# Performance work log

Hardware: AMD Instinct MI355X
Metric: run time of the kernel (lower is better)

The kernel has to match this reference:

```python
import jax, jax.numpy as jnp
import numpy as np
import math

# dims
BSZ, L, D = 2, 4096, 1024
EXPAND, DS, NH, NG, DC, CS = 2, 128, 32, 1, 4, 64
DI = EXPAND * D            # 2048
HP = DI // NH              # 64 headdim
D_IN_PROJ = 2 * DI + 2 * NG * DS + NH  # 4384
CONV_DIM = DI + 2 * NG * DS            # 2304
EPS = 1e-5


def setup_inputs() -> dict:
    key = jax.random.key(0)
    ks = jax.random.split(key, 10)
    u = jax.random.normal(ks[0], (BSZ, L, D), dtype=jnp.float32)
    W_in = jax.random.normal(ks[1], (D, D_IN_PROJ), dtype=jnp.float32) / math.sqrt(D)
    conv_w = jax.random.normal(ks[2], (CONV_DIM, DC), dtype=jnp.float32) / math.sqrt(DC)
    conv_b = jnp.zeros((CONV_DIM,), dtype=jnp.float32)
    # dt init as in module: dt ~ logspace(1e-3, 0.1), dt_bias = inv softplus
    dt = jnp.exp(jax.random.uniform(ks[3], (NH,)) * (math.log(0.1) - math.log(0.001)) + math.log(0.001))
    dt = jnp.clip(dt, 1e-4, None)
    dt_bias = dt + jnp.log(-jnp.expm1(-dt))
    A_log = jnp.log(jax.random.uniform(ks[4], (NH,), minval=1.0, maxval=16.0))
    norm_w = jnp.ones((DI,), dtype=jnp.float32)
    norm_b = jnp.zeros((DI,), dtype=jnp.float32)
    W_out = jax.random.normal(ks[5], (DI, D), dtype=jnp.float32) / math.sqrt(DI)
    return {"u": u, "W_in": W_in, "conv_w": conv_w, "conv_b": conv_b,
            "dt_bias": dt_bias, "A_log": A_log, "norm_w": norm_w,
            "norm_b": norm_b, "W_out": W_out}


def _segsum(x):
    # x: (..., l) -> (..., l, l), out[i,j] = sum_{j<t<=i} x[t], -inf above diag
    cs = jnp.cumsum(x, axis=-1)
    d = cs[..., :, None] - cs[..., None, :]
    n = x.shape[-1]
    mask = jnp.tril(jnp.ones((n, n), dtype=bool))
    return jnp.where(mask, d, -jnp.inf)


def _ssd(x, A, Bm, Cm):
    # x: (b,l,h,p) already scaled by dt; A: (b,l,h) = a*dt; Bm,Cm: (b,l,h,n)
    b, l, h, p = x.shape
    nc = l // CS
    x = x.reshape(b, nc, CS, h, p)
    A = A.reshape(b, nc, CS, h).transpose(0, 3, 1, 2)          # (b,h,c,s)
    Bm = Bm.reshape(b, nc, CS, h, -1)
    Cm = Cm.reshape(b, nc, CS, h, -1)
    A_cum = jnp.cumsum(A, axis=-1)                              # (b,h,c,s)
    Lmat = jnp.exp(_segsum(A))                                  # (b,h,c,s,s)
    # intra-chunk (diagonal block) output
    Yd = jnp.einsum('bclhn,bcshn,bhcls,bcshp->bclhp', Cm, Bm, Lmat, x)
    # per-chunk final states
    decay_states = jnp.exp(A_cum[..., -1:] - A_cum)             # (b,h,c,s)
    states = jnp.einsum('bcshn,bhcs,bcshp->bchpn', Bm, decay_states, x)
    # inter-chunk recurrence (parallel via segsum over chunk decays)
    A_chunk = jnp.pad(A_cum[..., -1], ((0, 0), (0, 0), (1, 0)))  # (b,h,c+1)
    decay_chunk = jnp.exp(_segsum(A_chunk))                      # (b,h,c+1,c+1)
    states0 = jnp.concatenate([jnp.zeros_like(states[:, :1]), states], axis=1)
    new_states = jnp.einsum('bhzc,bchpn->bzhpn', decay_chunk, states0)
    states_in = new_states[:, :-1]                               # (b,c,h,p,n)
    state_decay = jnp.exp(A_cum)                                 # (b,h,c,s)
    Yoff = jnp.einsum('bcshn,bchpn,bhcs->bcshp', Cm, states_in, state_decay)
    return (Yd + Yoff).reshape(b, l, h, p)


def _causal_dwconv(x, w, b):
    # x: (B,L,C), depthwise causal conv, kernel w: (C,K), bias b: (C,)
    k = w.shape[1]
    xp = jnp.pad(x, ((0, 0), (k - 1, 0), (0, 0)))
    seqlen = x.shape[1]
    out = b
    for i in range(k):  # small fixed kernel loop (K=4)
        out = out + xp[:, i:i + seqlen, :] * w[:, i]
    return out


def reference(u, W_in, conv_w, conv_b, dt_bias, A_log, norm_w, norm_b, W_out):
    b, l, _ = u.shape
    zxbcdt = u @ W_in                                  # (b,l,2*DI+2*NG*DS+NH)
    z = zxbcdt[..., :DI]
    xBC = zxbcdt[..., DI:DI + CONV_DIM]
    dt = jax.nn.softplus(zxbcdt[..., -NH:] + dt_bias)  # (b,l,h)
    A = -jnp.exp(A_log)                                # (h,)
    xBC = jax.nn.silu(_causal_dwconv(xBC, conv_w, conv_b))
    x = xBC[..., :DI].reshape(b, l, NH, HP)
    Bv = xBC[..., DI:DI + NG * DS].reshape(b, l, NG, DS)
    Cv = xBC[..., DI + NG * DS:].reshape(b, l, NG, DS)
    # broadcast groups to heads
    rep = NH // NG
    Bh = jnp.repeat(Bv, rep, axis=2)                   # (b,l,h,n)
    Ch = jnp.repeat(Cv, rep, axis=2)
    y = _ssd(x * dt[..., None], A * dt, Bh, Ch)        # (b,l,h,p)
    y = y.reshape(b, l, DI)
    y = y * jax.nn.silu(z)                             # gated
    mu = jnp.mean(y, axis=-1, keepdims=True)
    var = jnp.mean(jnp.square(y - mu), axis=-1, keepdims=True)
    y = (y - mu) * jax.lax.rsqrt(var + EPS) * norm_w + norm_b
    return y @ W_out
```

## Files before the change

kernel.cpp:

```cpp
#include <hip/hip_runtime.h>
#include <hip/hip_bf16.h>
#include <math.h>


namespace {

constexpr int kB   = 2;
constexpr int kL   = 4096;
constexpr int kDI  = 2048;
constexpr int kDS  = 128;
constexpr int kNH  = 32;
constexpr int kHP  = 64;
constexpr int kDC  = 4;
constexpr int kCS  = 64;
constexpr int kNC  = kL / kCS;
constexpr int kDProj   = 2 * kDI + 2 * kDS + kNH;
constexpr int kDProjP  = 4480;
constexpr int kConvDim = kDI + 2 * kDS;
constexpr int kRows = kB * kL;
constexpr float kEps = 1e-5f;
constexpr int kTS = 136;
constexpr int kWS = 72;

typedef __bf16 bf16x8 __attribute__((ext_vector_type(8)));
typedef float f32x4 __attribute__((ext_vector_type(4)));
typedef unsigned short ushort8 __attribute__((ext_vector_type(8)));

__device__ inline float bu2f(unsigned short u) {
  union { unsigned int i; float f; } x; x.i = ((unsigned int)u) << 16; return x.f;
}
__device__ inline unsigned short f2bu(float f) {
  __hip_bfloat16 h = __float2bfloat16(f);
  return *reinterpret_cast<unsigned short*>(&h);
}

__device__ inline void store_out(float* C, size_t i, float v) { C[i] = v; }
__device__ inline void store_out(unsigned short* C, size_t i, float v) { C[i] = f2bu(v); }

__device__ inline void gld_lds16(const unsigned short* g, unsigned short* l) {
  __builtin_amdgcn_global_load_lds(
      (const __attribute__((address_space(1))) unsigned int*)g,
      (__attribute__((address_space(3))) unsigned int*)l, 16, 0, 0);
}

__global__ void cast_kernel(const float4* __restrict__ in, ushort4* __restrict__ out, int n4) {
  int i = blockIdx.x * 256 + threadIdx.x;
  if (i >= n4) return;
  float4 v = in[i];
  ushort4 o;
  o.x = f2bu(v.x); o.y = f2bu(v.y); o.z = f2bu(v.z); o.w = f2bu(v.w);
  out[i] = o;
}

__global__ void transpose_cast(const float* __restrict__ in, unsigned short* __restrict__ out,
                               int R, int C, const float* __restrict__ scale) {
  __shared__ float t[32][33];
  const int c0 = blockIdx.x * 32;
  const int r0 = blockIdx.y * 32;
  const int tx = threadIdx.x & 31, ty = threadIdx.x >> 5;
  for (int rr = ty; rr < 32; rr += 8) {
    int c = c0 + tx;
    float v = (c < C) ? in[(size_t)(r0 + rr) * C + c] : 0.f;
    if (scale) v *= scale[r0 + rr];
    t[rr][tx] = v;
  }
  __syncthreads();
  for (int cc = ty; cc < 32; cc += 8) {
    int orow = c0 + cc;
    out[(size_t)orow * R + r0 + tx] = f2bu(t[tx][cc]);
  }
}

__global__ void colsum_kernel(const float* __restrict__ W2, const float* __restrict__ wv,
                              const float* __restrict__ bv,
                              float* __restrict__ t1, float* __restrict__ t2) {
  __shared__ float p1[4][64], p2[4][64];
  const int nl = threadIdx.x & 63;
  const int ks = threadIdx.x >> 6;
  const int n = blockIdx.x * 64 + nl;
  float s1 = 0.f, s2 = 0.f;
  for (int k = ks * 512; k < ks * 512 + 512; k++) {
    float v = W2[(size_t)k * 1024 + n];
    s1 += wv[k] * v;
    s2 += bv[k] * v;
  }
  p1[ks][nl] = s1; p2[ks][nl] = s2;
  __syncthreads();
  if (threadIdx.x < 64) {
    t1[blockIdx.x * 64 + threadIdx.x] =
        p1[0][threadIdx.x] + p1[1][threadIdx.x] + p1[2][threadIdx.x] + p1[3][threadIdx.x];
    t2[blockIdx.x * 64 + threadIdx.x] =
        p2[0][threadIdx.x] + p2[1][threadIdx.x] + p2[2][threadIdx.x] + p2[3][threadIdx.x];
  }
}

template <typename OutT, bool FOLD>
__global__ __launch_bounds__(256) void gemm_bt(const unsigned short* __restrict__ A,
                                               const unsigned short* __restrict__ Bt,
                                               OutT* __restrict__ C, int M, int N, int K,
                                               const float* __restrict__ mu,
                                               const float* __restrict__ rstd,
                                               const float* __restrict__ t1,
                                               const float* __restrict__ t2) {
  __shared__ __align__(16) unsigned short As[128 * 32];
  __shared__ __align__(16) unsigned short Bs[128 * 32];
  const int tid = threadIdx.x;
  const int wave = tid >> 6, lane = tid & 63;
  const int m0 = blockIdx.y * 128, n0 = blockIdx.x * 128;
  const int wr = (wave >> 1) * 64, wc = (wave & 1) * 64;
  const int st_row = lane >> 2;
  const int st_col = (((lane & 3) ^ ((st_row >> 1) & 3))) * 8;
  const unsigned short* pA[2];
  const unsigned short* pB[2];
  unsigned short* lA[2];
  unsigned short* lB[2];
#pragma unroll
  for (int r = 0; r < 2; r++) {
    int q = wave * 2 + r;
    pA[r] = A + (size_t)(m0 + q * 16 + st_row) * K + st_col;
    pB[r] = Bt + (size_t)(n0 + q * 16 + st_row) * K + st_col;
    lA[r] = &As[q * 512];
    lB[r] = &Bs[q * 512];
  }
  const int frag_row = lane & 15;
  const int rk = (((lane >> 4) ^ ((frag_row >> 1) & 3))) * 8;
  f32x4 acc[4][4] = {};
  for (int k0 = 0; k0 < K; k0 += 32) {
#pragma unroll
    for (int r = 0; r < 2; r++) {
      gld_lds16(pA[r] + k0, lA[r]);
      gld_lds16(pB[r] + k0, lB[r]);
    }
    asm volatile("s_waitcnt vmcnt(0)" ::: "memory");
    __syncthreads();
    bf16x8 af[4], bfr[4];
#pragma unroll
    for (int i = 0; i < 4; i++)
      af[i] = *(const bf16x8*)&As[(wr + i * 16 + frag_row) * 32 + rk];
#pragma unroll
    for (int j = 0; j < 4; j++)
      bfr[j] = *(const bf16x8*)&Bs[(wc + j * 16 + frag_row) * 32 + rk];
#pragma unroll
    for (int i = 0; i < 4; i++)
#pragma unroll
      for (int j = 0; j < 4; j++)
        acc[i][j] = __builtin_amdgcn_mfma_f32_16x16x32_bf16(af[i], bfr[j], acc[i][j], 0, 0, 0);
    __syncthreads();
  }
  const int crow = (lane >> 4) * 4;
  const int ccol = lane & 15;
#pragma unroll
  for (int i = 0; i < 4; i++) {
#pragma unroll
    for (int j = 0; j < 4; j++) {
      int n = n0 + wc + j * 16 + ccol;
      if (n < N) {
        float c1 = FOLD ? t1[n] : 0.f;
        float c2 = FOLD ? t2[n] : 0.f;
#pragma unroll
        for (int r = 0; r < 4; r++) {
          int m = m0 + wr + i * 16 + crow + r;
          float v = acc[i][j][r];
          if (FOLD) v = rstd[m] * (v - mu[m] * c1) + c2;
          store_out(C, (size_t)m * N + n, v);
        }
      }
    }
  }
}

__global__ void dt_kernel(const unsigned short* __restrict__ zxbcdt,
                          const float* __restrict__ dt_bias,
                          float* __restrict__ dtbuf) {
  int idx = blockIdx.x * 256 + threadIdx.x;
  if (idx >= kRows * kNH) return;
  int row = idx >> 5, h = idx & 31;
  float x = bu2f(zxbcdt[(size_t)row * kDProj + (kDProj - kNH) + h]) + dt_bias[h];
  dtbuf[idx] = (x > 15.f) ? x : log1pf(expf(x));
}

__global__ void conv_silu_kernel(const unsigned short* __restrict__ zxbcdt,
                                 const float* __restrict__ conv_w,
                                 const float* __restrict__ conv_b,
                                 unsigned short* __restrict__ xbc_act) {
  int c = blockIdx.x * 256 + threadIdx.x;
  if (c >= kConvDim) return;
  const int r0 = blockIdx.y * 8;
  const int l0 = r0 & (kL - 1);
  const float w0 = conv_w[c * 4], w1 = conv_w[c * 4 + 1];
  const float w2 = conv_w[c * 4 + 2], w3 = conv_w[c * 4 + 3];
  const float bias = conv_b[c];
  float v[11];
#pragma unroll
  for (int i = 0; i < 11; i++) {
    int l = l0 - 3 + i;
    v[i] = (l >= 0) ? bu2f(zxbcdt[(size_t)(r0 - 3 + i) * kDProj + kDI + c]) : 0.f;
  }
#pragma unroll
  for (int j = 0; j < 8; j++) {
    float a = bias + v[j] * w0 + v[j + 1] * w1 + v[j + 2] * w2 + v[j + 3] * w3;
    xbc_act[(size_t)(r0 + j) * kConvDim + c] = f2bu(a / (1.f + expf(-a)));
  }
}

__global__ __launch_bounds__(256) void chunk_state_kernel(
    const unsigned short* __restrict__ xbc_act,
    const float* __restrict__ dtbuf,
    const float* __restrict__ A_log,
    unsigned short* __restrict__ states,
    float* __restrict__ asum) {
  const int id = blockIdx.x;
  const int h = id & 31;
  const int c = (id >> 5) & (kNC - 1);
  const int b = id >> 11;
  const int tid = threadIdx.x;
  const int wave = tid >> 6, lane = tid & 63;
  __shared__ __align__(16) unsigned short sBT[kDS * kWS];
  __shared__ __align__(16) unsigned short sxd[kCS * kWS];
  __shared__ float s_dt[kCS];
  __shared__ float s_acum[kCS];
  const int l0 = b * kL + c * kCS;
  if (tid < kCS) s_dt[tid] = dtbuf[(size_t)(l0 + tid) * kNH + h];
  __syncthreads();
  if (tid == 0) {
    float A = -expf(A_log[h]);
    float run = 0.f;
    for (int s = 0; s < kCS; s++) { run += A * s_dt[s]; s_acum[s] = run; }
    asum[id] = run;
  }
  __syncthreads();
  const float total = s_acum[kCS - 1];
  for (int e = tid; e < kCS * kDS; e += 256) {
    int s = e >> 7, n = e & 127;
    sBT[n * kWS + s] = xbc_act[(size_t)(l0 + s) * kConvDim + kDI + n];
  }
  for (int e = tid; e < kCS * kHP; e += 256) {
    int s = e >> 6, p = e & 63;
    float xv = bu2f(xbc_act[(size_t)(l0 + s) * kConvDim + h * kHP + p]);
    sxd[p * kWS + s] = f2bu(xv * s_dt[s] * expf(total - s_acum[s]));
  }
  __syncthreads();
  const int arow = wave * 16 + (lane & 15);
  const int fk = (lane >> 4) * 8;
  f32x4 acc[8] = {};
#pragma unroll
  for (int kk = 0; kk < 2; kk++) {
    bf16x8 a = *(const bf16x8*)&sxd[arow * kWS + kk * 32 + fk];
#pragma unroll
    for (int j = 0; j < 8; j++) {
      bf16x8 bb = *(const bf16x8*)&sBT[(j * 16 + (lane & 15)) * kWS + kk * 32 + fk];
      acc[j] = __builtin_amdgcn_mfma_f32_16x16x32_bf16(a, bb, acc[j], 0, 0, 0);
    }
  }
  const int prow = wave * 16 + (lane >> 4) * 4;
  const int ncol = lane & 15;
  size_t base = (size_t)id * (kHP * kDS);
#pragma unroll
  for (int j = 0; j < 8; j++)
#pragma unroll
    for (int r = 0; r < 4; r++)
      states[base + (size_t)(prow + r) * kDS + j * 16 + ncol] = f2bu(acc[j][r]);
}

__global__ void scan_kernel(unsigned short* __restrict__ states,
                            const float* __restrict__ asum) {
  const int blk = blockIdx.x;
  const int seg = blk & 7;
  const int bh = blk >> 3;
  const int h = bh & 31, b = bh >> 5;
  const int e4 = seg * 256 + threadIdx.x;
  float c0 = 0.f, c1 = 0.f, c2 = 0.f, c3 = 0.f;
  for (int c = 0; c < kNC; c++) {
    const int id = (b * kNC + c) * kNH + h;
    ushort4* p = (ushort4*)states + (size_t)id * 2048 + e4;
    float decay = expf(asum[id]);
    ushort4 t = *p;
    ushort4 o;
    o.x = f2bu(c0); o.y = f2bu(c1); o.z = f2bu(c2); o.w = f2bu(c3);
    *p = o;
    c0 = c0 * decay + bu2f(t.x);
    c1 = c1 * decay + bu2f(t.y);
    c2 = c2 * decay + bu2f(t.z);
    c3 = c3 * decay + bu2f(t.w);
  }
}

__global__ __launch_bounds__(256) void y_kernel(
    const unsigned short* __restrict__ xbc_act,
    const unsigned short* __restrict__ zxbcdt,
    const unsigned short* __restrict__ states_in,
    const float* __restrict__ dtbuf,
    const float* __restrict__ A_log,
    unsigned short* __restrict__ ybuf,
    float* __restrict__ pS, float* __restrict__ pQ) {
  const int id = blockIdx.x;
  const int hg = id & 7;
  const int c = (id >> 3) & (kNC - 1);
  const int b = id >> 9;
  const int tid = threadIdx.x;
  const int wave = tid >> 6, lane = tid & 63;
  __shared__ __align__(16) unsigned short sC[kCS * kTS];
  __shared__ __align__(16) unsigned short sB[kCS * kTS];
  __shared__ __align__(16) unsigned short sxd[kCS * kWS];
  __shared__ __align__(16) unsigned short sW[kCS * kWS];
  __shared__ float s_dt[4][kCS];
  __shared__ float s_acum[4][kCS];
  const int l0 = b * kL + c * kCS;
  {
    int hh = tid >> 6, s = tid & 63;
    s_dt[hh][s] = dtbuf[(size_t)(l0 + s) * kNH + hg * 4 + hh];
  }
  __syncthreads();
  if (tid < 4) {
    float A = -expf(A_log[hg * 4 + tid]);
    float run = 0.f;
    for (int s = 0; s < kCS; s++) { run += A * s_dt[tid][s]; s_acum[tid][s] = run; }
  }
  for (int e = tid; e < kCS * 16; e += 256) {
    int row = e >> 4, c8 = (e & 15) * 8;
    size_t rb = (size_t)(l0 + row) * kConvDim;
    *(ushort8*)&sB[row * kTS + c8] = *(const ushort8*)&xbc_act[rb + kDI + c8];
    *(ushort8*)&sC[row * kTS + c8] = *(const ushort8*)&xbc_act[rb + kDI + kDS + c8];
  }
  __syncthreads();
  const int arow = wave * 16 + (lane & 15);
  const int fk = (lane >> 4) * 8;
  f32x4 accG[4] = {};
#pragma unroll
  for (int kk = 0; kk < 4; kk++) {
    bf16x8 a = *(const bf16x8*)&sC[arow * kTS + kk * 32 + fk];
#pragma unroll
    for (int j = 0; j < 4; j++) {
      bf16x8 bb = *(const bf16x8*)&sB[(j * 16 + (lane & 15)) * kTS + kk * 32 + fk];
      accG[j] = __builtin_amdgcn_mfma_f32_16x16x32_bf16(a, bb, accG[j], 0, 0, 0);
    }
  }
  const int lrow = wave * 16 + (lane >> 4) * 4;
  const size_t sbase = (size_t)((b * kNC + c) * kNH) * (kHP * kDS);
  float rS[4] = {}, rQ[4] = {};
  for (int hh = 0; hh < 4; hh++) {
    const int h = hg * 4 + hh;
    __syncthreads();
    for (int e = tid; e < kCS * kHP; e += 256) {
      int s = e >> 6, p = e & 63;
      float xv = bu2f(xbc_act[(size_t)(l0 + s) * kConvDim + h * kHP + p]);
      sxd[p * kWS + s] = f2bu(xv * s_dt[hh][s]);
    }
#pragma unroll
    for (int j = 0; j < 4; j++) {
      int scol = j * 16 + (lane & 15);
      float as = s_acum[hh][scol];
#pragma unroll
      for (int r = 0; r < 4; r++) {
        int l = lrow + r;
        float w = (scol <= l) ? accG[j][r] * expf(s_acum[hh][l] - as) : 0.f;
        sW[l * kWS + scol] = f2bu(w);
      }
    }
    for (int e = tid; e < kCS * 16; e += 256) {
      int row = e >> 4, c8 = (e & 15) * 8;
      *(ushort8*)&sB[row * kTS + c8] =
          *(const ushort8*)&states_in[sbase + (size_t)h * (kHP * kDS) + row * kDS + c8];
    }
    __syncthreads();
    f32x4 accY[4] = {};
#pragma unroll
    for (int kk = 0; kk < 2; kk++) {
      bf16x8 a = *(const bf16x8*)&sW[arow * kWS + kk * 32 + fk];
#pragma unroll
      for (int j = 0; j < 4; j++) {
        bf16x8 bb = *(const bf16x8*)&sxd[(j * 16 + (lane & 15)) * kWS + kk * 32 + fk];
        accY[j] = __builtin_amdgcn_mfma_f32_16x16x32_bf16(a, bb, accY[j], 0, 0, 0);
      }
    }
    f32x4 accO[4] = {};
#pragma unroll
    for (int kk = 0; kk < 4; kk++) {
      bf16x8 a = *(const bf16x8*)&sC[arow * kTS + kk * 32 + fk];
#pragma unroll
      for (int j = 0; j < 4; j++) {
        bf16x8 bb = *(const bf16x8*)&sB[(j * 16 + (lane & 15)) * kTS + kk * 32 + fk];
        accO[j] = __builtin_amdgcn_mfma_f32_16x16x32_bf16(a, bb, accO[j], 0, 0, 0);
      }
    }
#pragma unroll
    for (int r = 0; r < 4; r++) {
      int l = lrow + r;
      float el = expf(s_acum[hh][l]);
      size_t zrow = (size_t)(l0 + l) * kDProj + h * kHP;
      size_t yrow = (size_t)(l0 + l) * kDI + h * kHP;
#pragma unroll
      for (int j = 0; j < 4; j++) {
        int p = j * 16 + (lane & 15);
        float yv = accY[j][r] + el * accO[j][r];
        float z = bu2f(zxbcdt[zrow + p]);
        yv *= z / (1.f + expf(-z));
        rS[r] += yv;
        rQ[r] += yv * yv;
        ybuf[yrow + p] = f2bu(yv);
      }
    }
  }
#pragma unroll
  for (int m = 1; m < 16; m <<= 1) {
#pragma unroll
    for (int r = 0; r < 4; r++) {
      rS[r] += __shfl_xor(rS[r], m);
      rQ[r] += __shfl_xor(rQ[r], m);
    }
  }
  if ((lane & 15) == 0) {
#pragma unroll
    for (int r = 0; r < 4; r++) {
      int row = l0 + lrow + r;
      pS[(size_t)row * 8 + hg] = rS[r];
      pQ[(size_t)row * 8 + hg] = rQ[r];
    }
  }
}

__global__ void ln_reduce(const float* __restrict__ pS, const float* __restrict__ pQ,
                          float* __restrict__ mu, float* __restrict__ rstd) {
  int row = blockIdx.x * 256 + threadIdx.x;
  if (row >= kRows) return;
  float s = 0.f, q = 0.f;
#pragma unroll
  for (int i = 0; i < 8; i++) { s += pS[(size_t)row * 8 + i]; q += pQ[(size_t)row * 8 + i]; }
  float m = s / kDI;
  mu[row] = m;
  rstd[row] = rsqrtf(q / kDI - m * m + kEps);
}

}

extern "C" void kernel_launch(void* const* d_in, const int* in_sizes, int n_in,
                              void* d_out, int out_size, void* d_ws, size_t ws_size,
                              hipStream_t stream) {
  const float* u       = (const float*)d_in[0];
  const float* W_in    = (const float*)d_in[1];
  const float* conv_w  = (const float*)d_in[2];
  const float* conv_b  = (const float*)d_in[3];
  const float* dt_bias = (const float*)d_in[4];
  const float* A_log   = (const float*)d_in[5];
  const float* norm_w  = (const float*)d_in[6];
  const float* norm_b  = (const float*)d_in[7];
  const float* W_out   = (const float*)d_in[8];
  float* out = (float*)d_out;

  char* ws = (char*)d_ws;
  size_t off = 0;
  auto alloc = [&](size_t bytes) {
    void* p = ws + off;
    off += (bytes + 255) & ~(size_t)255;
    return p;
  };
  unsigned short* zxbcdt = (unsigned short*)alloc((size_t)kRows * kDProj * 2);
  unsigned short* xbc    = (unsigned short*)alloc((size_t)kRows * kConvDim * 2);
  float* dtb             = (float*)alloc((size_t)kRows * kNH * 4);
  float* asum            = (float*)alloc((size_t)kB * kNC * kNH * 4);
  unsigned short* A1     = (unsigned short*)alloc((size_t)kRows * 1024 * 2);
  unsigned short* Bt1    = (unsigned short*)alloc((size_t)kDProjP * 1024 * 2);
  unsigned short* states = (unsigned short*)alloc((size_t)kB * kNC * kNH * kHP * kDS * 2);
  unsigned short* Bt2    = (unsigned short*)alloc((size_t)1024 * kDI * 2);
  unsigned short* ybuf   = (unsigned short*)alloc((size_t)kRows * kDI * 2);
  float* mu              = (float*)alloc((size_t)kRows * 4);
  float* rstd            = (float*)alloc((size_t)kRows * 4);
  float* t1              = (float*)alloc(1024 * 4);
  float* t2              = (float*)alloc(1024 * 4);
  float* pS              = (float*)alloc((size_t)kRows * 8 * 4);
  float* pQ              = (float*)alloc((size_t)kRows * 8 * 4);
  (void)ws_size; (void)in_sizes; (void)n_in; (void)out_size;

  cast_kernel<<<(kRows * 1024 / 4 + 255) / 256, 256, 0, stream>>>(
      (const float4*)u, (ushort4*)A1, kRows * 1024 / 4);
  transpose_cast<<<dim3(kDProjP / 32, 1024 / 32), 256, 0, stream>>>(
      W_in, Bt1, 1024, kDProj, nullptr);
  transpose_cast<<<dim3(1024 / 32, 2048 / 32), 256, 0, stream>>>(
      W_out, Bt2, 2048, 1024, norm_w);
  colsum_kernel<<<16, 256, 0, stream>>>(W_out, norm_w, norm_b, t1, t2);
  gemm_bt<unsigned short, false><<<dim3(kDProjP / 128, kRows / 128), 256, 0, stream>>>(
      A1, Bt1, zxbcdt, kRows, kDProj, 1024, nullptr, nullptr, nullptr, nullptr);
  dt_kernel<<<(kRows * kNH + 255) / 256, 256, 0, stream>>>(zxbcdt, dt_bias, dtb);
  conv_silu_kernel<<<dim3((kConvDim + 255) / 256, kRows / 8), 256, 0, stream>>>(
      zxbcdt, conv_w, conv_b, xbc);
  chunk_state_kernel<<<kB * kNC * kNH, 256, 0, stream>>>(xbc, dtb, A_log, states, asum);
  scan_kernel<<<kB * kNH * 8, 256, 0, stream>>>(states, asum);
  y_kernel<<<kB * kNC * 8, 256, 0, stream>>>(xbc, zxbcdt, states, dtb, A_log, ybuf, pS, pQ);
  ln_reduce<<<kRows / 256, 256, 0, stream>>>(pS, pQ, mu, rstd);
  gemm_bt<float, true><<<dim3(1024 / 128, kRows / 128), 256, 0, stream>>>(
      ybuf, Bt2, out, kRows, 1024, 2048, mu, rstd, t1, t2);
}
```

Before: 457.7 us.

## Fuse prep kernels, dt softplus and LN reduce into GEMMs; vectorize conv; prefetch scan

Merges the cast, two transposes and the column-sum into a single prep launch. Folds the dt softplus into the input-projection GEMM epilogue and the LayerNorm row reduction into the output GEMM prologue, which removes three launches. The causal conv now handles four channels per thread with vector loads. The scan prefetches the next chunk's state and decay, and y_kernel reads inter-chunk states straight from global memory instead of staging them in LDS. In exchange, the prep kernel's branchy block dispatch and the uncached global B-fragment reads in y_kernel may cost bandwidth.

Result: slower. 575.0 us (+25.6%).

```diff
diff --git a/kernel.cpp b/kernel.cpp
--- a/kernel.cpp
+++ b/kernel.cpp
@@ -43,21 +43,12 @@
       (__attribute__((address_space(3))) unsigned int*)l, 16, 0, 0);
 }
 
-__global__ void cast_kernel(const float4* __restrict__ in, ushort4* __restrict__ out, int n4) {
-  int i = blockIdx.x * 256 + threadIdx.x;
-  if (i >= n4) return;
-  float4 v = in[i];
-  ushort4 o;
-  o.x = f2bu(v.x); o.y = f2bu(v.y); o.z = f2bu(v.z); o.w = f2bu(v.w);
-  out[i] = o;
-}
-
-__global__ void transpose_cast(const float* __restrict__ in, unsigned short* __restrict__ out,
-                               int R, int C, const float* __restrict__ scale) {
-  __shared__ float t[32][33];
-  const int c0 = blockIdx.x * 32;
-  const int r0 = blockIdx.y * 32;
-  const int tx = threadIdx.x & 31, ty = threadIdx.x >> 5;
+__device__ void do_transpose(const float* __restrict__ in, unsigned short* __restrict__ out,
+                             int R, int C, const float* __restrict__ scale,
+                             int bx, int by, int tid, float (*t)[33]) {
+  const int c0 = bx * 32;
+  const int r0 = by * 32;
+  const int tx = tid & 31, ty = tid >> 5;
   for (int rr = ty; rr < 32; rr += 8) {
     int c = c0 + tx;
     float v = (c < C) ? in[(size_t)(r0 + rr) * C + c] : 0.f;
@@ -71,42 +62,81 @@
   }
 }
 
-__global__ void colsum_kernel(const float* __restrict__ W2, const float* __restrict__ wv,
-                              const float* __restrict__ bv,
-                              float* __restrict__ t1, float* __restrict__ t2) {
-  __shared__ float p1[4][64], p2[4][64];
-  const int nl = threadIdx.x & 63;
-  const int ks = threadIdx.x >> 6;
-  const int n = blockIdx.x * 64 + nl;
-  float s1 = 0.f, s2 = 0.f;
-  for (int k = ks * 512; k < ks * 512 + 512; k++) {
-    float v = W2[(size_t)k * 1024 + n];
-    s1 += wv[k] * v;
-    s2 += bv[k] * v;
-  }
-  p1[ks][nl] = s1; p2[ks][nl] = s2;
-  __syncthreads();
-  if (threadIdx.x < 64) {
-    t1[blockIdx.x * 64 + threadIdx.x] =
-        p1[0][threadIdx.x] + p1[1][threadIdx.x] + p1[2][threadIdx.x] + p1[3][threadIdx.x];
-    t2[blockIdx.x * 64 + threadIdx.x] =
-        p2[0][threadIdx.x] + p2[1][threadIdx.x] + p2[2][threadIdx.x] + p2[3][threadIdx.x];
-  }
-}
-
-template <typename OutT, bool FOLD>
+__global__ void prep_kernel(const float* __restrict__ u, unsigned short* __restrict__ A1,
+                            const float* __restrict__ W_in, unsigned short* __restrict__ Bt1,
+                            const float* __restrict__ W_out, unsigned short* __restrict__ Bt2,
+                            const float* __restrict__ norm_w, const float* __restrict__ norm_b,
+                            float* __restrict__ t1, float* __restrict__ t2) {
+  __shared__ __align__(16) char smem[32 * 33 * 4];
+  int blk = blockIdx.x;
+  const int tid = threadIdx.x;
+  if (blk < 8192) {
+    int i = blk * 256 + tid;
+    float4 v = ((const float4*)u)[i];
+    ushort4 o;
+    o.x = f2bu(v.x); o.y = f2bu(v.y); o.z = f2bu(v.z); o.w = f2bu(v.w);
+    ((ushort4*)A1)[i] = o;
+    return;
+  }
+  blk -= 8192;
+  if (blk < 140 * 32) {
+    do_transpose(W_in, Bt1, 1024, kDProj, nullptr, blk % 140, blk / 140, tid,
+                 (float(*)[33])smem);
+    return;
+  }
+  blk -= 140 * 32;
+  if (blk < 32 * 64) {
+    do_transpose(W_out, Bt2, 2048, 1024, norm_w, blk % 32, blk / 32, tid,
+                 (float(*)[33])smem);
+    return;
+  }
+  blk -= 32 * 64;
+  {
+    float* p1 = (float*)smem;
+    float* p2 = p1 + 256;
+    const int nl = tid & 63;
+    const int ks = tid >> 6;
+    const int n = blk * 64 + nl;
+    float s1 = 0.f, s2 = 0.f;
+    for (int k = ks * 512; k < ks * 512 + 512; k++) {
+      float v = W_out[(size_t)k * 1024 + n];
+      s1 += norm_w[k] * v;
+      s2 += norm_b[k] * v;
+    }
+    p1[ks * 64 + nl] = s1; p2[ks * 64 + nl] = s2;
+    __syncthreads();
+    if (tid < 64) {
+      t1[blk * 64 + tid] = p1[tid] + p1[64 + tid] + p1[128 + tid] + p1[192 + tid];
+      t2[blk * 64 + tid] = p2[tid] + p2[64 + tid] + p2[128 + tid] + p2[192 + tid];
+    }
+  }
+}
+
+template <typename OutT, bool FOLD, bool DT>
 __global__ __launch_bounds__(256) void gemm_bt(const unsigned short* __restrict__ A,
                                                const unsigned short* __restrict__ Bt,
                                                OutT* __restrict__ C, int M, int N, int K,
-                                               const float* __restrict__ mu,
-                                               const float* __restrict__ rstd,
+                                               const float* __restrict__ pS,
+                                               const float* __restrict__ pQ,
                                                const float* __restrict__ t1,
-                                               const float* __restrict__ t2) {
+                                               const float* __restrict__ t2,
+                                               const float* __restrict__ dt_bias,
+                                               float* __restrict__ dtbuf) {
   __shared__ __align__(16) unsigned short As[128 * 32];
   __shared__ __align__(16) unsigned short Bs[128 * 32];
+  __shared__ float smu[128], srstd[128];
   const int tid = threadIdx.x;
   const int wave = tid >> 6, lane = tid & 63;
   const int m0 = blockIdx.y * 128, n0 = blockIdx.x * 128;
+  if (FOLD && tid < 128) {
+    int row = m0 + tid;
+    float s = 0.f, q = 0.f;
+#pragma unroll
+    for (int i = 0; i < 8; i++) { s += pS[(size_t)row * 8 + i]; q += pQ[(size_t)row * 8 + i]; }
+    float m = s / kDI;
+    smu[tid] = m;
+    srstd[tid] = rsqrtf(q / kDI - m * m + kEps);
+  }
   const int wr = (wave >> 1) * 64, wc = (wave & 1) * 64;
   const int st_row = lane >> 2;
   const int st_col = (((lane & 3) ^ ((st_row >> 1) & 3))) * 8;
@@ -157,49 +187,62 @@
       if (n < N) {
         float c1 = FOLD ? t1[n] : 0.f;
         float c2 = FOLD ? t2[n] : 0.f;
+        bool isdt = DT && (n >= N - kNH);
+        float db = isdt ? dt_bias[n - (N - kNH)] : 0.f;
 #pragma unroll
         for (int r = 0; r < 4; r++) {
           int m = m0 + wr + i * 16 + crow + r;
           float v = acc[i][j][r];
-          if (FOLD) v = rstd[m] * (v - mu[m] * c1) + c2;
+          if (FOLD) v = srstd[m - m0] * (v - smu[m - m0] * c1) + c2;
           store_out(C, (size_t)m * N + n, v);
+          if (isdt) {
+            float x = acc[i][j][r] + db;
+            dtbuf[(size_t)m * kNH + (n - (N - kNH))] = (x > 15.f) ? x : log1pf(expf(x));
+          }
         }
       }
     }
   }
-}
-
-__global__ void dt_kernel(const unsigned short* __restrict__ zxbcdt,
-                          const float* __restrict__ dt_bias,
-                          float* __restrict__ dtbuf) {
-  int idx = blockIdx.x * 256 + threadIdx.x;
-  if (idx >= kRows * kNH) return;
-  int row = idx >> 5, h = idx & 31;
-  float x = bu2f(zxbcdt[(size_t)row * kDProj + (kDProj - kNH) + h]) + dt_bias[h];
-  dtbuf[idx] = (x > 15.f) ? x : log1pf(expf(x));
 }
 
 __global__ void conv_silu_kernel(const unsigned short* __restrict__ zxbcdt,
                                  const float* __restrict__ conv_w,
                                  const float* __restrict__ conv_b,
                                  unsigned short* __restrict__ xbc_act) {
-  int c = blockIdx.x * 256 + threadIdx.x;
-  if (c >= kConvDim) return;
+  int c4 = blockIdx.x * 256 + threadIdx.x;
+  if (c4 >= kConvDim / 4) return;
+  const int c = c4 * 4;
   const int r0 = blockIdx.y * 8;
   const int l0 = r0 & (kL - 1);
-  const float w0 = conv_w[c * 4], w1 = conv_w[c * 4 + 1];
-  const float w2 = conv_w[c * 4 + 2], w3 = conv_w[c * 4 + 3];
-  const float bias = conv_b[c];
-  float v[11];
+  float4 w[4];
+  float bias[4];
+#pragma unroll
+  for (int q = 0; q < 4; q++) {
+    w[q] = ((const float4*)conv_w)[c + q];
+    bias[q] = conv_b[c + q];
+  }
+  float v[11][4];
 #pragma unroll
   for (int i = 0; i < 11; i++) {
     int l = l0 - 3 + i;
-    v[i] = (l >= 0) ? bu2f(zxbcdt[(size_t)(r0 - 3 + i) * kDProj + kDI + c]) : 0.f;
+    if (l >= 0) {
+      ushort4 t = *(const ushort4*)&zxbcdt[(size_t)(r0 - 3 + i) * kDProj + kDI + c];
+      v[i][0] = bu2f(t.x); v[i][1] = bu2f(t.y); v[i][2] = bu2f(t.z); v[i][3] = bu2f(t.w);
+    } else {
+      v[i][0] = v[i][1] = v[i][2] = v[i][3] = 0.f;
+    }
   }
 #pragma unroll
   for (int j = 0; j < 8; j++) {
-    float a = bias + v[j] * w0 + v[j + 1] * w1 + v[j + 2] * w2 + v[j + 3] * w3;
-    xbc_act[(size_t)(r0 + j) * kConvDim + c] = f2bu(a / (1.f + expf(-a)));
+    ushort4 o;
+    unsigned short* op = (unsigned short*)&o;
+#pragma unroll
+    for (int q = 0; q < 4; q++) {
+      float a = bias[q] + v[j][q] * w[q].x + v[j + 1][q] * w[q].y +
+                v[j + 2][q] * w[q].z + v[j + 3][q] * w[q].w;
+      op[q] = f2bu(a / (1.f + expf(-a)));
+    }
+    *(ushort4*)&xbc_act[(size_t)(r0 + j) * kConvDim + c] = o;
   }
 }
 
@@ -269,19 +312,27 @@
   const int bh = blk >> 3;
   const int h = bh & 31, b = bh >> 5;
   const int e4 = seg * 256 + threadIdx.x;
+  const size_t cstride = (size_t)kNH * 2048;
+  ushort4* p = (ushort4*)states + ((size_t)(b * kNC) * kNH + h) * 2048 + e4;
+  const float* ap = asum + (b * kNC) * kNH + h;
   float c0 = 0.f, c1 = 0.f, c2 = 0.f, c3 = 0.f;
+  ushort4 t = p[0];
+  float dec = expf(ap[0]);
   for (int c = 0; c < kNC; c++) {
-    const int id = (b * kNC + c) * kNH + h;
-    ushort4* p = (ushort4*)states + (size_t)id * 2048 + e4;
-    float decay = expf(asum[id]);
-    ushort4 t = *p;
+    ushort4 tn = t;
+    float decn = dec;
+    if (c + 1 < kNC) {
+      tn = p[(size_t)(c + 1) * cstride];
+      decn = expf(ap[(c + 1) * kNH]);
+    }
     ushort4 o;
     o.x = f2bu(c0); o.y = f2bu(c1); o.z = f2bu(c2); o.w = f2bu(c3);
-    *p = o;
-    c0 = c0 * decay + bu2f(t.x);
-    c1 = c1 * decay + bu2f(t.y);
-    c2 = c2 * decay + bu2f(t.z);
-    c3 = c3 * decay + bu2f(t.w);
+    p[(size_t)c * cstride] = o;
+    c0 = c0 * dec + bu2f(t.x);
+    c1 = c1 * dec + bu2f(t.y);
+    c2 = c2 * dec + bu2f(t.z);
+    c3 = c3 * dec + bu2f(t.w);
+    t = tn; dec = decn;
   }
 }
 
@@ -357,11 +408,6 @@
         sW[l * kWS + scol] = f2bu(w);
       }
     }
-    for (int e = tid; e < kCS * 16; e += 256) {
-      int row = e >> 4, c8 = (e & 15) * 8;
-      *(ushort8*)&sB[row * kTS + c8] =
-          *(const ushort8*)&states_in[sbase + (size_t)h * (kHP * kDS) + row * kDS + c8];
-    }
     __syncthreads();
     f32x4 accY[4] = {};
 #pragma unroll
@@ -373,13 +419,14 @@
         accY[j] = __builtin_amdgcn_mfma_f32_16x16x32_bf16(a, bb, accY[j], 0, 0, 0);
       }
     }
+    const unsigned short* sin_h = states_in + sbase + (size_t)h * (kHP * kDS);
     f32x4 accO[4] = {};
 #pragma unroll
     for (int kk = 0; kk < 4; kk++) {
       bf16x8 a = *(const bf16x8*)&sC[arow * kTS + kk * 32 + fk];
 #pragma unroll
       for (int j = 0; j < 4; j++) {
-        bf16x8 bb = *(const bf16x8*)&sB[(j * 16 + (lane & 15)) * kTS + kk * 32 + fk];
+        bf16x8 bb = *(const bf16x8*)&sin_h[(size_t)(j * 16 + (lane & 15)) * kDS + kk * 32 + fk];
         accO[j] = __builtin_amdgcn_mfma_f32_16x16x32_bf16(a, bb, accO[j], 0, 0, 0);
       }
     }
@@ -417,18 +464,6 @@
       pQ[(size_t)row * 8 + hg] = rQ[r];
     }
   }
-}
-
-__global__ void ln_reduce(const float* __restrict__ pS, const float* __restrict__ pQ,
-                          float* __restrict__ mu, float* __restrict__ rstd) {
-  int row = blockIdx.x * 256 + threadIdx.x;
-  if (row >= kRows) return;
-  float s = 0.f, q = 0.f;
-#pragma unroll
-  for (int i = 0; i < 8; i++) { s += pS[(size_t)row * 8 + i]; q += pQ[(size_t)row * 8 + i]; }
-  float m = s / kDI;
-  mu[row] = m;
-  rstd[row] = rsqrtf(q / kDI - m * m + kEps);
 }
 
 }
@@ -463,30 +498,20 @@
   unsigned short* states = (unsigned short*)alloc((size_t)kB * kNC * kNH * kHP * kDS * 2);
   unsigned short* Bt2    = (unsigned short*)alloc((size_t)1024 * kDI * 2);
   unsigned short* ybuf   = (unsigned short*)alloc((size_t)kRows * kDI * 2);
-  float* mu              = (float*)alloc((size_t)kRows * 4);
-  float* rstd            = (float*)alloc((size_t)kRows * 4);
   float* t1              = (float*)alloc(1024 * 4);
   float* t2              = (float*)alloc(1024 * 4);
   float* pS              = (float*)alloc((size_t)kRows * 8 * 4);
   float* pQ              = (float*)alloc((size_t)kRows * 8 * 4);
   (void)ws_size; (void)in_sizes; (void)n_in; (void)out_size;
 
-  cast_kernel<<<(kRows * 1024 / 4 + 255) / 256, 256, 0, stream>>>(
-      (const float4*)u, (ushort4*)A1, kRows * 1024 / 4);
-  transpose_cast<<<dim3(kDProjP / 32, 1024 / 32), 256, 0, stream>>>(
-      W_in, Bt1, 1024, kDProj, nullptr);
-  transpose_cast<<<dim3(1024 / 32, 2048 / 32), 256, 0, stream>>>(
-      W_out, Bt2, 2048, 1024, norm_w);
-  colsum_kernel<<<16, 256, 0, stream>>>(W_out, norm_w, norm_b, t1, t2);
-  gemm_bt<unsigned short, false><<<dim3(kDProjP / 128, kRows / 128), 256, 0, stream>>>(
-      A1, Bt1, zxbcdt, kRows, kDProj, 1024, nullptr, nullptr, nullptr, nullptr);
-  dt_kernel<<<(kRows * kNH + 255) / 256, 256, 0, stream>>>(zxbcdt, dt_bias, dtb);
-  conv_silu_kernel<<<dim3((kConvDim + 255) / 256, kRows / 8), 256, 0, stream>>>(
-      zxbcdt, conv_w, conv_b, xbc);
+  prep_kernel<<<8192 + 140 * 32 + 32 * 64 + 16, 256, 0, stream>>>(
+      u, A1, W_in, Bt1, W_out, Bt2, norm_w, norm_b, t1, t2);
+  gemm_bt<unsigned short, false, true><<<dim3(kDProjP / 128, kRows / 128), 256, 0, stream>>>(
+      A1, Bt1, zxbcdt, kRows, kDProj, 1024, nullptr, nullptr, nullptr, nullptr, dt_bias, dtb);
+  conv_silu_kernel<<<dim3(3, kRows / 8), 256, 0, stream>>>(zxbcdt, conv_w, conv_b, xbc);
   chunk_state_kernel<<<kB * kNC * kNH, 256, 0, stream>>>(xbc, dtb, A_log, states, asum);
   scan_kernel<<<kB * kNH * 8, 256, 0, stream>>>(states, asum);
   y_kernel<<<kB * kNC * 8, 256, 0, stream>>>(xbc, zxbcdt, states, dtb, A_log, ybuf, pS, pQ);
-  ln_reduce<<<kRows / 256, 256, 0, stream>>>(pS, pQ, mu, rstd);
-  gemm_bt<float, true><<<dim3(1024 / 128, kRows / 128), 256, 0, stream>>>(
-      ybuf, Bt2, out, kRows, 1024, 2048, mu, rstd, t1, t2);
-}
+  gemm_bt<float, true, false><<<dim3(1024 / 128, kRows / 128), 256, 0, stream>>>(
+      ybuf, Bt2, out, kRows, 1024, 2048, pS, pQ, t1, t2, nullptr, nullptr);
+}
```
